# Kernel tuning notes

Measured on AMD Instinct MI355X. Metric: run time of the kernel, lower is better.

The kernel has to match this reference:

```python
import jax, jax.numpy as jnp
import numpy as np

N_LIG, N_TGT, E = 100000, 4000, 150000
D_LIG, D_TGT, H = 4, 1280, 128


def _seg_mean(feat, idx, n):
    # segment mean; isolated nodes get 0 (PyG mean aggr semantics)
    s = jax.ops.segment_sum(feat, idx, num_segments=n)
    c = jax.ops.segment_sum(jnp.ones((idx.shape[0], 1), feat.dtype), idx, num_segments=n)
    return s / jnp.maximum(c, 1.0)


def setup_inputs() -> dict:
    key = jax.random.key(0)
    ks = jax.random.split(key, 20)
    s = 0.05  # weight scale
    inp = {
        'x_ligand': jax.random.normal(ks[0], (N_LIG, D_LIG), jnp.float32),
        'x_target': jax.random.normal(ks[1], (N_TGT, D_TGT), jnp.float32),
        'edge_index': jnp.stack([
            jax.random.randint(ks[2], (E,), 0, N_LIG, jnp.int32),
            jax.random.randint(ks[3], (E,), 0, N_TGT, jnp.int32),
        ]),
        'W1lt_l': jax.random.normal(ks[4], (D_LIG, H), jnp.float32) * s,
        'b1lt':   jax.random.normal(ks[5], (H,), jnp.float32) * s,
        'W1lt_r': jax.random.normal(ks[6], (D_TGT, H), jnp.float32) * s,
        'W1tl_l': jax.random.normal(ks[7], (D_TGT, H), jnp.float32) * s,
        'b1tl':   jax.random.normal(ks[8], (H,), jnp.float32) * s,
        'W1tl_r': jax.random.normal(ks[9], (D_LIG, H), jnp.float32) * s,
        'W2lt_l': jax.random.normal(ks[10], (H, H), jnp.float32) * s,
        'b2lt':   jax.random.normal(ks[11], (H,), jnp.float32) * s,
        'W2lt_r': jax.random.normal(ks[12], (H, H), jnp.float32) * s,
        'W2tl_l': jax.random.normal(ks[13], (H, H), jnp.float32) * s,
        'b2tl':   jax.random.normal(ks[14], (H,), jnp.float32) * s,
        'W2tl_r': jax.random.normal(ks[15], (H, H), jnp.float32) * s,
        'Wp':     jax.random.normal(ks[16], (2 * H, 1), jnp.float32) * s,
        'bp':     jax.random.normal(ks[17], (1,), jnp.float32) * s,
    }
    return inp


def reference(x_ligand, x_target, edge_index,
              W1lt_l, b1lt, W1lt_r, W1tl_l, b1tl, W1tl_r,
              W2lt_l, b2lt, W2lt_r, W2tl_l, b2tl, W2tl_r, Wp, bp):
    src, dst = edge_index[0], edge_index[1]  # ligand idx, target idx

    # conv1: SAGEConv  out = lin_l(mean_j x_src[j]) + lin_r(x_dst)
    m_t = _seg_mean(x_ligand[src], dst, N_TGT)              # [N_TGT, D_LIG]
    h_t = m_t @ W1lt_l + b1lt + x_target @ W1lt_r           # [N_TGT, H]
    m_l = _seg_mean(x_target[dst], src, N_LIG)              # [N_LIG, D_TGT]
    h_l = m_l @ W1tl_l + b1tl + x_ligand @ W1tl_r           # [N_LIG, H]
    h_t = jax.nn.relu(h_t)
    h_l = jax.nn.relu(h_l)

    # conv2 (hidden -> hidden), same edge structure
    m_t2 = _seg_mean(h_l[src], dst, N_TGT)
    h_t2 = jax.nn.relu(m_t2 @ W2lt_l + b2lt + h_t @ W2lt_r)
    m_l2 = _seg_mean(h_t[dst], src, N_LIG)
    h_l2 = jax.nn.relu(m_l2 @ W2tl_l + b2tl + h_l @ W2tl_r)

    # edge predictor: gather-cat-linear
    edge_feats = jnp.concatenate([h_l2[src], h_t2[dst]], axis=-1)  # [E, 2H]
    out = (edge_feats @ Wp + bp).squeeze(-1)                        # [E]
    return out
```

## Files before the change

### kernel.cpp

```cpp
#include <hip/hip_runtime.h>
#include <hip/hip_bf16.h>

#define N_LIG 100000
#define N_TGT 4000
#define NEDGE 150000
#define DT 1280
#define HD 128
#define CAP_L 32
#define CAP_T 128
#define NTILE_L 6250
#define PL_BLOCKS 1563

typedef __attribute__((ext_vector_type(8))) short short8v;
typedef __attribute__((ext_vector_type(4))) float f32x4;

static __device__ __forceinline__ ushort f2bf(float f) {
    __hip_bfloat16 h = __float2bfloat16(f);
    union { __hip_bfloat16 h; ushort u; } c; c.h = h; return c.u;
}
static __device__ __forceinline__ float bf2f(ushort u) {
    union { unsigned v; float f; } c; c.v = ((unsigned)u) << 16; return c.f;
}

__global__ __launch_bounds__(256) void k_pack(
    const float* __restrict__ W2, uint4* __restrict__ Wf,
    const float* __restrict__ Wr, const float* __restrict__ Wl,
    uint4* __restrict__ Wf1,
    const float* __restrict__ xt, uint4* __restrict__ xtf,
    int4* __restrict__ cntz,
    const float* __restrict__ W2a, const float* __restrict__ W2b,
    uint4* __restrict__ Wf2)
{
    int bx = blockIdx.x;
    if (bx < 8) {
        int gid = bx * 256 + threadIdx.x;
        int lane = gid & 63, frag = gid >> 6;
        int ks = frag >> 3, ct = frag & 7;
        int l15 = lane & 15, g = lane >> 4;
        int k = ks * 32 + g * 4, n = ct * 16 + l15;
        union { ushort us[8]; uint4 u; } o;
#pragma unroll
        for (int j = 0; j < 4; ++j) {
            o.us[j]     = f2bf(W2[(size_t)(k + j) * HD + n]);
            o.us[4 + j] = f2bf(W2[(size_t)(k + 16 + j) * HD + n]);
        }
        Wf[gid] = o.u;
    } else if (bx < 168) {
        int gid = (bx - 8) * 256 + threadIdx.x;
        int lane = gid & 63, frag = gid >> 6;
        int ks = frag >> 4, nct = frag & 15;
        int l15 = lane & 15, g = lane >> 4;
        int k = ks * 32 + g * 4, n = nct * 16 + l15;
        const float* Ws = (n < HD) ? Wr : Wl;
        int nn = n & 127;
        union { ushort us[8]; uint4 u; } o;
#pragma unroll
        for (int j = 0; j < 4; ++j) {
            o.us[j]     = f2bf(Ws[(size_t)(k + j) * HD + nn]);
            o.us[4 + j] = f2bf(Ws[(size_t)(k + 16 + j) * HD + nn]);
        }
        Wf1[gid] = o.u;
    } else if (bx < 2668) {
        int gid = (bx - 168) * 256 + threadIdx.x;
        int lane = gid & 63, frag = gid >> 6;
        int ks = frag % 40, rt = frag / 40;
        int row = rt * 16 + (lane & 15);
        int kb = ks * 32 + (lane >> 4) * 4;
        float4 a0 = *reinterpret_cast<const float4*>(xt + (size_t)row * DT + kb);
        float4 a1 = *reinterpret_cast<const float4*>(xt + (size_t)row * DT + kb + 16);
        union { ushort us[8]; uint4 u; } o;
        o.us[0] = f2bf(a0.x); o.us[1] = f2bf(a0.y); o.us[2] = f2bf(a0.z); o.us[3] = f2bf(a0.w);
        o.us[4] = f2bf(a1.x); o.us[5] = f2bf(a1.y); o.us[6] = f2bf(a1.z); o.us[7] = f2bf(a1.w);
        xtf[gid] = o.u;
    } else if (bx < 2770) {
        int i = (bx - 2668) * 256 + threadIdx.x;
        if (i < 26000) cntz[i] = make_int4(0, 0, 0, 0);
    } else {
        int gid = (bx - 2770) * 256 + threadIdx.x;
        int lane = gid & 63, frag = gid >> 6;
        int ks = frag >> 4, nct = frag & 15;
        int l15 = lane & 15, g = lane >> 4;
        int k = ks * 32 + g * 4, n = nct * 16 + l15;
        const float* Ws = (n < HD) ? W2a : W2b;
        int nn = n & 127;
        union { ushort us[8]; uint4 u; } o;
#pragma unroll
        for (int j = 0; j < 4; ++j) {
            o.us[j]     = f2bf(Ws[(size_t)(k + j) * HD + nn]);
            o.us[4 + j] = f2bf(Ws[(size_t)(k + 16 + j) * HD + nn]);
        }
        Wf2[gid] = o.u;
    }
}

__global__ __launch_bounds__(256) void k_fill(
    const int* __restrict__ src, const int* __restrict__ dst,
    int* __restrict__ cnt_src, int* __restrict__ cnt_dst,
    int* __restrict__ bsrc, int* __restrict__ bdst)
{
    int e = blockIdx.x * 256 + threadIdx.x;
    if (e >= NEDGE) return;
    int s = src[e], d = dst[e];
    int ps = atomicAdd(&cnt_src[s], 1);
    if (ps < CAP_L) bsrc[(size_t)s * CAP_L + ps] = d;
    int pd = atomicAdd(&cnt_dst[d], 1);
    if (pd < CAP_T) bdst[(size_t)d * CAP_T + pd] = s;
}

__global__ __launch_bounds__(512) void k_tgt1m(
    const uint4* __restrict__ xtf,
    const uint4* __restrict__ Wf1,
    const uint4* __restrict__ Wf2,
    const float* __restrict__ xl,
    const int* __restrict__ bdst, const int* __restrict__ cnt_dst,
    const float* __restrict__ W1lt_l,
    const float* __restrict__ b1lt,
    float* __restrict__ y_t1,
    float* __restrict__ y_t2, float* __restrict__ htW2r)
{
    __shared__ float  ms[16][4];
    __shared__ ushort hts[16][136];

    int w = threadIdx.x >> 6;
    int lane = threadIdx.x & 63;
    int l15 = lane & 15, g = lane >> 4;
    int rt = blockIdx.x;
    int row0 = rt * 16;

    if (threadIdx.x < 128) {
        int r = threadIdx.x >> 3, lane8 = threadIdx.x & 7;
        int row = row0 + r;
        int deg = cnt_dst[row];
        int n = min(deg, CAP_T);
        float4 acc = make_float4(0.f, 0.f, 0.f, 0.f);
        for (int i = lane8; i < n; i += 8) {
            int sid = bdst[(size_t)row * CAP_T + i];
            float4 x = *reinterpret_cast<const float4*>(xl + 4ull * (unsigned)sid);
            acc.x += x.x; acc.y += x.y; acc.z += x.z; acc.w += x.w;
        }
#pragma unroll
        for (int off = 1; off < 8; off <<= 1) {
            acc.x += __shfl_xor(acc.x, off); acc.y += __shfl_xor(acc.y, off);
            acc.z += __shfl_xor(acc.z, off); acc.w += __shfl_xor(acc.w, off);
        }
        if (lane8 == 0) {
            float dinv = 1.0f / fmaxf((float)deg, 1.0f);
            ms[r][0] = acc.x * dinv; ms[r][1] = acc.y * dinv;
            ms[r][2] = acc.z * dinv; ms[r][3] = acc.w * dinv;
        }
    }

    f32x4 acc[2];
#pragma unroll
    for (int ct = 0; ct < 2; ++ct) acc[ct] = (f32x4){0.f, 0.f, 0.f, 0.f};

    for (int ks = 0; ks < DT / 32; ++ks) {
        union { uint4 u; short8v s; } ua;
        ua.u = xtf[(size_t)(rt * 40 + ks) * 64 + lane];
#pragma unroll
        for (int ct = 0; ct < 2; ++ct) {
            union { uint4 u; short8v s; } ub;
            ub.u = Wf1[(size_t)(ks * 16 + w * 2 + ct) * 64 + lane];
            acc[ct] = __builtin_amdgcn_mfma_f32_16x16x32_bf16(ua.s, ub.s, acc[ct], 0, 0, 0);
        }
    }

    __syncthreads();

    if (w < 4) {
#pragma unroll
        for (int ct = 0; ct < 2; ++ct) {
            int c = w * 32 + ct * 16 + l15;
            float wl0 = W1lt_l[c], wl1 = W1lt_l[HD + c],
                  wl2 = W1lt_l[2 * HD + c], wl3 = W1lt_l[3 * HD + c];
            float bb = b1lt[c];
#pragma unroll
            for (int j = 0; j < 4; ++j) {
                int r = 4 * g + j;
                float v = acc[ct][j] + bb + ms[r][0] * wl0 + ms[r][1] * wl1
                        + ms[r][2] * wl2 + ms[r][3] * wl3;
                hts[r][c] = f2bf(fmaxf(v, 0.0f));
            }
        }
    } else {
#pragma unroll
        for (int ct = 0; ct < 2; ++ct) {
            int c = (w - 4) * 32 + ct * 16 + l15;
#pragma unroll
            for (int j = 0; j < 4; ++j) {
                int grow = row0 + 4 * g + j;
                y_t1[(size_t)grow * HD + c] = acc[ct][j];
            }
        }
    }
    __syncthreads();

    f32x4 acc2[2];
#pragma unroll
    for (int ct = 0; ct < 2; ++ct) acc2[ct] = (f32x4){0.f, 0.f, 0.f, 0.f};

#pragma unroll
    for (int ks2 = 0; ks2 < 4; ++ks2) {
        int kb2 = ks2 * 32 + g * 4;
        union { ushort us[8]; short8v s; } ua2;
        *reinterpret_cast<ushort4*>(&ua2.us[0]) =
            *reinterpret_cast<const ushort4*>(&hts[l15][kb2]);
        *reinterpret_cast<ushort4*>(&ua2.us[4]) =
            *reinterpret_cast<const ushort4*>(&hts[l15][kb2 + 16]);
#pragma unroll
        for (int ct = 0; ct < 2; ++ct) {
            union { uint4 u; short8v s; } ub2;
            ub2.u = Wf2[(size_t)(ks2 * 16 + w * 2 + ct) * 64 + lane];
            acc2[ct] = __builtin_amdgcn_mfma_f32_16x16x32_bf16(ua2.s, ub2.s, acc2[ct], 0, 0, 0);
        }
    }

    float* outp = (w < 4) ? y_t2 : htW2r;
    int cw = (w < 4) ? w : (w - 4);
#pragma unroll
    for (int ct = 0; ct < 2; ++ct) {
        int c = cw * 32 + ct * 16 + l15;
#pragma unroll
        for (int j = 0; j < 4; ++j) {
            int grow = row0 + 4 * g + j;
            outp[(size_t)grow * HD + c] = acc2[ct][j];
        }
    }
}

__global__ __launch_bounds__(256) void k_hl(
    const float* __restrict__ xl,
    const float* __restrict__ y_t1, const float* __restrict__ y_t2,
    const int* __restrict__ bsrc, const int* __restrict__ cnt_src,
    const float* __restrict__ W1tl_r,
    const float* __restrict__ b1tl,
    uint4* __restrict__ hlb,
    uint4* __restrict__ gl2)
{
    int tc = threadIdx.x & 15;
    int node = blockIdx.x * 16 + (threadIdx.x >> 4);
    int ks = tc >> 2, g = tc & 3;
    int kb = ks * 32 + g * 4;

    int deg = cnt_src[node];
    int n = min(deg, CAP_L);
    float4 s0 = make_float4(0.f, 0.f, 0.f, 0.f);
    float4 s1 = make_float4(0.f, 0.f, 0.f, 0.f);
    float4 t0 = make_float4(0.f, 0.f, 0.f, 0.f);
    float4 t1 = make_float4(0.f, 0.f, 0.f, 0.f);
    for (int i = 0; i < n; ++i) {
        int did = bsrc[(size_t)node * CAP_L + i];
        float4 v0 = *reinterpret_cast<const float4*>(y_t1 + (size_t)did * HD + kb);
        float4 v1 = *reinterpret_cast<const float4*>(y_t1 + (size_t)did * HD + kb + 16);
        float4 u0 = *reinterpret_cast<const float4*>(y_t2 + (size_t)did * HD + kb);
        float4 u1 = *reinterpret_cast<const float4*>(y_t2 + (size_t)did * HD + kb + 16);
        s0.x += v0.x; s0.y += v0.y; s0.z += v0.z; s0.w += v0.w;
        s1.x += v1.x; s1.y += v1.y; s1.z += v1.z; s1.w += v1.w;
        t0.x += u0.x; t0.y += u0.y; t0.z += u0.z; t0.w += u0.w;
        t1.x += u1.x; t1.y += u1.y; t1.z += u1.z; t1.w += u1.w;
    }
    float dinv = 1.0f / fmaxf((float)deg, 1.0f);
    float4 x = *reinterpret_cast<const float4*>(xl + 4ull * (unsigned)node);

    float4 b0 = *reinterpret_cast<const float4*>(b1tl + kb);
    float4 b1 = *reinterpret_cast<const float4*>(b1tl + kb + 16);
    float4 wa0 = *reinterpret_cast<const float4*>(W1tl_r + 0 * HD + kb);
    float4 wa1 = *reinterpret_cast<const float4*>(W1tl_r + 1 * HD + kb);
    float4 wa2 = *reinterpret_cast<const float4*>(W1tl_r + 2 * HD + kb);
    float4 wa3 = *reinterpret_cast<const float4*>(W1tl_r + 3 * HD + kb);
    float4 wb0 = *reinterpret_cast<const float4*>(W1tl_r + 0 * HD + kb + 16);
    float4 wb1 = *reinterpret_cast<const float4*>(W1tl_r + 1 * HD + kb + 16);
    float4 wb2 = *reinterpret_cast<const float4*>(W1tl_r + 2 * HD + kb + 16);
    float4 wb3 = *reinterpret_cast<const float4*>(W1tl_r + 3 * HD + kb + 16);

    union { ushort us[8]; uint4 u; } o;
    o.us[0] = f2bf(fmaxf(s0.x * dinv + b0.x + x.x * wa0.x + x.y * wa1.x + x.z * wa2.x + x.w * wa3.x, 0.f));
    o.us[1] = f2bf(fmaxf(s0.y * dinv + b0.y + x.x * wa0.y + x.y * wa1.y + x.z * wa2.y + x.w * wa3.y, 0.f));
    o.us[2] = f2bf(fmaxf(s0.z * dinv + b0.z + x.x * wa0.z + x.y * wa1.z + x.z * wa2.z + x.w * wa3.z, 0.f));
    o.us[3] = f2bf(fmaxf(s0.w * dinv + b0.w + x.x * wa0.w + x.y * wa1.w + x.z * wa2.w + x.w * wa3.w, 0.f));
    o.us[4] = f2bf(fmaxf(s1.x * dinv + b1.x + x.x * wb0.x + x.y * wb1.x + x.z * wb2.x + x.w * wb3.x, 0.f));
    o.us[5] = f2bf(fmaxf(s1.y * dinv + b1.y + x.x * wb0.y + x.y * wb1.y + x.z * wb2.y + x.w * wb3.y, 0.f));
    o.us[6] = f2bf(fmaxf(s1.z * dinv + b1.z + x.x * wb0.z + x.y * wb1.z + x.z * wb2.z + x.w * wb3.z, 0.f));
    o.us[7] = f2bf(fmaxf(s1.w * dinv + b1.w + x.x * wb0.w + x.y * wb1.w + x.z * wb2.w + x.w * wb3.w, 0.f));
    hlb[(size_t)node * 16 + tc] = o.u;

    union { ushort us[8]; uint4 u; } q;
    q.us[0] = f2bf(t0.x * dinv); q.us[1] = f2bf(t0.y * dinv);
    q.us[2] = f2bf(t0.z * dinv); q.us[3] = f2bf(t0.w * dinv);
    q.us[4] = f2bf(t1.x * dinv); q.us[5] = f2bf(t1.y * dinv);
    q.us[6] = f2bf(t1.z * dinv); q.us[7] = f2bf(t1.w * dinv);
    gl2[(size_t)node * 16 + tc] = q.u;
}

__global__ __launch_bounds__(256) void k_ptl(
    const uint4* __restrict__ hlb,
    const uint4* __restrict__ Wf,
    const ushort* __restrict__ gl2,
    const int* __restrict__ bdst, const int* __restrict__ cnt_dst,
    const float* __restrict__ Wlt,
    const float* __restrict__ b2lt,
    const float* __restrict__ b2tl,
    const float* __restrict__ htW2r,
    const float* __restrict__ Wp,
    float* __restrict__ p_t, float* __restrict__ p_l)
{
    __shared__ int   idx[CAP_T];
    __shared__ float sm[16][132];
    __shared__ float msh[HD];
    __shared__ float sum2[2];

    if (blockIdx.x < N_TGT) {
        int row = blockIdx.x;
        int deg = cnt_dst[row];
        int nn = min(deg, CAP_T);

        if (threadIdx.x < CAP_T) idx[threadIdx.x] = bdst[(size_t)row * CAP_T + threadIdx.x];
        __syncthreads();

        int wg = threadIdx.x >> 4, l16 = threadIdx.x & 15;
        float s[8];
#pragma unroll
        for (int j = 0; j < 8; ++j) s[j] = 0.f;
        for (int i = wg; i < nn; i += 16) {
            int sid = idx[i];
            union { uint4 u; ushort us[8]; } v;
            v.u = hlb[(size_t)sid * 16 + l16];
#pragma unroll
            for (int j = 0; j < 8; ++j) s[j] += bf2f(v.us[j]);
        }
#pragma unroll
        for (int j = 0; j < 8; ++j) sm[wg][l16 * 8 + j] = s[j];
        __syncthreads();

        if (threadIdx.x < HD) {
            int h = threadIdx.x;
            int tc2 = h >> 3, jj = h & 7;
            float dinv = 1.0f / fmaxf((float)deg, 1.0f);
            float acc = 0.f;
#pragma unroll
            for (int w2 = 0; w2 < 16; ++w2) acc += sm[w2][tc2 * 8 + jj];
            int ks2 = tc2 >> 2, g2 = tc2 & 3;
            int col = ks2 * 32 + ((jj >> 2) << 4) + g2 * 4 + (jj & 3);
            msh[col] = acc * dinv;
        }
        __syncthreads();

        if (threadIdx.x < HD) {
            int h = threadIdx.x;
            float g = 0.f;
            for (int k = 0; k < HD; k += 4) {
                float4 mk = *reinterpret_cast<const float4*>(&msh[k]);
                g += mk.x * Wlt[(size_t)(k + 0) * HD + h] + mk.y * Wlt[(size_t)(k + 1) * HD + h]
                   + mk.z * Wlt[(size_t)(k + 2) * HD + h] + mk.w * Wlt[(size_t)(k + 3) * HD + h];
            }
            float v = fmaxf(g + b2lt[h] + htW2r[(size_t)row * HD + h], 0.0f);
            float part = v * Wp[HD + h];
#pragma unroll
            for (int off = 1; off < 64; off <<= 1) part += __shfl_xor(part, off);
            if ((h & 63) == 0) sum2[h >> 6] = part;
        }
        __syncthreads();
        if (threadIdx.x == 0) p_t[row] = sum2[0] + sum2[1];
        return;
    }

    int wid = threadIdx.x >> 6;
    int lane = threadIdx.x & 63;
    int l15 = lane & 15, g = lane >> 4;
    int tile = (blockIdx.x - N_TGT) * 4 + wid;
    int wrow0 = tile * 16;

    int arow = wrow0 + l15;
    if (arow >= N_LIG) arow = N_LIG - 1;

    f32x4 acc[8];
#pragma unroll
    for (int ct = 0; ct < 8; ++ct) acc[ct] = (f32x4){0.f, 0.f, 0.f, 0.f};

#pragma unroll
    for (int ks = 0; ks < 4; ++ks) {
        union { uint4 u; short8v s; } ua;
        ua.u = hlb[(size_t)arow * 16 + ks * 4 + g];
#pragma unroll
        for (int ct = 0; ct < 8; ++ct) {
            union { uint4 u; short8v s; } ub;
            ub.u = Wf[(ks * 8 + ct) * 64 + lane];
            acc[ct] = __builtin_amdgcn_mfma_f32_16x16x32_bf16(ua.s, ub.s, acc[ct], 0, 0, 0);
        }
    }

    float wpv[8], bv[8];
    int off8[8];
#pragma unroll
    for (int ct = 0; ct < 8; ++ct) {
        int c = ct * 16 + l15;
        wpv[ct] = Wp[c];
        bv[ct]  = b2tl[c];
        off8[ct] = (((ct >> 1) * 4 + (l15 >> 2)) << 3) + ((ct & 1) << 2) + (l15 & 3);
    }

#pragma unroll
    for (int j = 0; j < 4; ++j) {
        int row = wrow0 + g * 4 + j;
        bool valid = row < N_LIG;
        int lrow = valid ? row : 0;
        const ushort* gp = gl2 + (size_t)lrow * HD;
        float part = 0.f;
#pragma unroll
        for (int ct = 0; ct < 8; ++ct) {
            float v = acc[ct][j] + bf2f(gp[off8[ct]]) + bv[ct];
            part += fmaxf(v, 0.f) * wpv[ct];
        }
#pragma unroll
        for (int off = 1; off < 16; off <<= 1) part += __shfl_xor(part, off);
        if (valid && l15 == 0) p_l[row] = part;
    }
}

__global__ __launch_bounds__(256) void k_out(
    const int* __restrict__ src, const int* __restrict__ dst,
    const float* __restrict__ p_l, const float* __restrict__ p_t,
    const float* __restrict__ bp, float* __restrict__ out)
{
    int e = blockIdx.x * 256 + threadIdx.x;
    if (e >= NEDGE) return;
    out[e] = p_l[src[e]] + p_t[dst[e]] + bp[0];
}

extern "C" void kernel_launch(void* const* d_in, const int* in_sizes, int n_in,
                              void* d_out, int out_size, void* d_ws, size_t ws_size,
                              hipStream_t stream)
{
    const float* x_l    = (const float*)d_in[0];
    const float* x_t    = (const float*)d_in[1];
    const int*   ei     = (const int*)  d_in[2];
    const float* W1lt_l = (const float*)d_in[3];
    const float* b1lt   = (const float*)d_in[4];
    const float* W1lt_r = (const float*)d_in[5];
    const float* W1tl_l = (const float*)d_in[6];
    const float* b1tl   = (const float*)d_in[7];
    const float* W1tl_r = (const float*)d_in[8];
    const float* W2lt_l = (const float*)d_in[9];
    const float* b2lt   = (const float*)d_in[10];
    const float* W2lt_r = (const float*)d_in[11];
    const float* W2tl_l = (const float*)d_in[12];
    const float* b2tl   = (const float*)d_in[13];
    const float* W2tl_r = (const float*)d_in[14];
    const float* Wp     = (const float*)d_in[15];
    const float* bp     = (const float*)d_in[16];

    const int* src = ei;
    const int* dst = ei + NEDGE;

    char* ws = (char*)d_ws;
    size_t o = 0;
    int* cnt_src = (int*)(ws + o); o += (size_t)N_LIG * 4;
    int* cnt_dst = (int*)(ws + o); o += (size_t)N_TGT * 4;
    int* bsrc = (int*)(ws + o); o += (size_t)N_LIG * CAP_L * 4;
    int* bdst = (int*)(ws + o); o += (size_t)N_TGT * CAP_T * 4;
    uint4* hlb   = (uint4*)(ws + o);  o += (size_t)N_LIG * HD * 2;
    uint4* gl2   = (uint4*)(ws + o);  o += (size_t)N_LIG * HD * 2;
    uint4* Wf    = (uint4*)(ws + o);  o += (size_t)32 * 64 * 16;
    uint4* Wf1   = (uint4*)(ws + o);  o += (size_t)640 * 64 * 16;
    uint4* Wf2   = (uint4*)(ws + o);  o += (size_t)64 * 64 * 16;
    uint4* xtf   = (uint4*)(ws + o);  o += (size_t)10000 * 64 * 16;
    float* y_t1  = (float*)(ws + o); o += (size_t)N_TGT * HD * 4;
    float* y_t2  = (float*)(ws + o); o += (size_t)N_TGT * HD * 4;
    float* htW2r = (float*)(ws + o); o += (size_t)N_TGT * HD * 4;
    float* p_l   = (float*)(ws + o); o += (size_t)N_LIG * 4;
    float* p_t   = (float*)(ws + o); o += (size_t)N_TGT * 4;

    float* out = (float*)d_out;

    k_pack<<<2786, 256, 0, stream>>>(W2tl_r, Wf, W1lt_r, W1tl_l, Wf1,
                                     x_t, xtf, (int4*)cnt_src,
                                     W2tl_l, W2lt_r, Wf2);

    k_fill<<<(NEDGE + 255) / 256, 256, 0, stream>>>(src, dst, cnt_src, cnt_dst, bsrc, bdst);

    k_tgt1m<<<N_TGT / 16, 512, 0, stream>>>(xtf, Wf1, Wf2, x_l, bdst, cnt_dst,
                                            W1lt_l, b1lt, y_t1, y_t2, htW2r);

    k_hl<<<NTILE_L, 256, 0, stream>>>(x_l, y_t1, y_t2, bsrc, cnt_src,
                                      W1tl_r, b1tl, hlb, gl2);

    k_ptl<<<N_TGT + PL_BLOCKS, 256, 0, stream>>>(hlb, Wf, (const ushort*)gl2,
                                                 bdst, cnt_dst,
                                                 W2lt_l, b2lt, b2tl, htW2r, Wp,
                                                 p_t, p_l);

    k_out<<<(NEDGE + 255) / 256, 256, 0, stream>>>(src, dst, p_l, p_t, bp, out);
}
```

Before: 107.6 us.

## Fuse ligand conv2 MFMA and predictor dot into the h_l aggregation kernel

The ligand-side conv2 matmul and edge-predictor projection now run in the same kernel that builds h_l and the gathered target mean. The 16-node tile is staged in shared memory and fed to the MFMA there, so the bf16 gl2 buffer is never written to or re-read from global memory. The target-side part moves to its own kernel. Each 16-row tile is now split across four waves by output columns, which needs an extra shared-memory reduction and barriers in a kernel that was previously pure gather.

```diff
diff --git a/kernel.cpp b/kernel.cpp
--- a/kernel.cpp
+++ b/kernel.cpp
@@ -9,7 +9,6 @@
 #define CAP_L 32
 #define CAP_T 128
 #define NTILE_L 6250
-#define PL_BLOCKS 1563
 
 typedef __attribute__((ext_vector_type(8))) short short8v;
 typedef __attribute__((ext_vector_type(4))) float f32x4;
@@ -228,193 +227,200 @@
     }
 }
 
-__global__ __launch_bounds__(256) void k_hl(
+__global__ __launch_bounds__(256) void k_hlp(
     const float* __restrict__ xl,
     const float* __restrict__ y_t1, const float* __restrict__ y_t2,
     const int* __restrict__ bsrc, const int* __restrict__ cnt_src,
     const float* __restrict__ W1tl_r,
     const float* __restrict__ b1tl,
+    const uint4* __restrict__ Wf,
+    const float* __restrict__ b2tl,
+    const float* __restrict__ Wp,
     uint4* __restrict__ hlb,
-    uint4* __restrict__ gl2)
-{
+    float* __restrict__ p_l)
+{
+    __shared__ uint4 Ah[16][17];
+    __shared__ uint4 Gh[16][17];
+    __shared__ float plp[4][16];
+
     int tc = threadIdx.x & 15;
-    int node = blockIdx.x * 16 + (threadIdx.x >> 4);
+    int nd = threadIdx.x >> 4;
+    int node = blockIdx.x * 16 + nd;
     int ks = tc >> 2, g = tc & 3;
     int kb = ks * 32 + g * 4;
 
-    int deg = cnt_src[node];
-    int n = min(deg, CAP_L);
-    float4 s0 = make_float4(0.f, 0.f, 0.f, 0.f);
-    float4 s1 = make_float4(0.f, 0.f, 0.f, 0.f);
-    float4 t0 = make_float4(0.f, 0.f, 0.f, 0.f);
-    float4 t1 = make_float4(0.f, 0.f, 0.f, 0.f);
-    for (int i = 0; i < n; ++i) {
-        int did = bsrc[(size_t)node * CAP_L + i];
-        float4 v0 = *reinterpret_cast<const float4*>(y_t1 + (size_t)did * HD + kb);
-        float4 v1 = *reinterpret_cast<const float4*>(y_t1 + (size_t)did * HD + kb + 16);
-        float4 u0 = *reinterpret_cast<const float4*>(y_t2 + (size_t)did * HD + kb);
-        float4 u1 = *reinterpret_cast<const float4*>(y_t2 + (size_t)did * HD + kb + 16);
-        s0.x += v0.x; s0.y += v0.y; s0.z += v0.z; s0.w += v0.w;
-        s1.x += v1.x; s1.y += v1.y; s1.z += v1.z; s1.w += v1.w;
-        t0.x += u0.x; t0.y += u0.y; t0.z += u0.z; t0.w += u0.w;
-        t1.x += u1.x; t1.y += u1.y; t1.z += u1.z; t1.w += u1.w;
-    }
-    float dinv = 1.0f / fmaxf((float)deg, 1.0f);
-    float4 x = *reinterpret_cast<const float4*>(xl + 4ull * (unsigned)node);
-
-    float4 b0 = *reinterpret_cast<const float4*>(b1tl + kb);
-    float4 b1 = *reinterpret_cast<const float4*>(b1tl + kb + 16);
-    float4 wa0 = *reinterpret_cast<const float4*>(W1tl_r + 0 * HD + kb);
-    float4 wa1 = *reinterpret_cast<const float4*>(W1tl_r + 1 * HD + kb);
-    float4 wa2 = *reinterpret_cast<const float4*>(W1tl_r + 2 * HD + kb);
-    float4 wa3 = *reinterpret_cast<const float4*>(W1tl_r + 3 * HD + kb);
-    float4 wb0 = *reinterpret_cast<const float4*>(W1tl_r + 0 * HD + kb + 16);
-    float4 wb1 = *reinterpret_cast<const float4*>(W1tl_r + 1 * HD + kb + 16);
-    float4 wb2 = *reinterpret_cast<const float4*>(W1tl_r + 2 * HD + kb + 16);
-    float4 wb3 = *reinterpret_cast<const float4*>(W1tl_r + 3 * HD + kb + 16);
-
-    union { ushort us[8]; uint4 u; } o;
-    o.us[0] = f2bf(fmaxf(s0.x * dinv + b0.x + x.x * wa0.x + x.y * wa1.x + x.z * wa2.x + x.w * wa3.x, 0.f));
-    o.us[1] = f2bf(fmaxf(s0.y * dinv + b0.y + x.x * wa0.y + x.y * wa1.y + x.z * wa2.y + x.w * wa3.y, 0.f));
-    o.us[2] = f2bf(fmaxf(s0.z * dinv + b0.z + x.x * wa0.z + x.y * wa1.z + x.z * wa2.z + x.w * wa3.z, 0.f));
-    o.us[3] = f2bf(fmaxf(s0.w * dinv + b0.w + x.x * wa0.w + x.y * wa1.w + x.z * wa2.w + x.w * wa3.w, 0.f));
-    o.us[4] = f2bf(fmaxf(s1.x * dinv + b1.x + x.x * wb0.x + x.y * wb1.x + x.z * wb2.x + x.w * wb3.x, 0.f));
-    o.us[5] = f2bf(fmaxf(s1.y * dinv + b1.y + x.x * wb0.y + x.y * wb1.y + x.z * wb2.y + x.w * wb3.y, 0.f));
-    o.us[6] = f2bf(fmaxf(s1.z * dinv + b1.z + x.x * wb0.z + x.y * wb1.z + x.z * wb2.z + x.w * wb3.z, 0.f));
-    o.us[7] = f2bf(fmaxf(s1.w * dinv + b1.w + x.x * wb0.w + x.y * wb1.w + x.z * wb2.w + x.w * wb3.w, 0.f));
-    hlb[(size_t)node * 16 + tc] = o.u;
-
-    union { ushort us[8]; uint4 u; } q;
-    q.us[0] = f2bf(t0.x * dinv); q.us[1] = f2bf(t0.y * dinv);
-    q.us[2] = f2bf(t0.z * dinv); q.us[3] = f2bf(t0.w * dinv);
-    q.us[4] = f2bf(t1.x * dinv); q.us[5] = f2bf(t1.y * dinv);
-    q.us[6] = f2bf(t1.z * dinv); q.us[7] = f2bf(t1.w * dinv);
-    gl2[(size_t)node * 16 + tc] = q.u;
-}
-
-__global__ __launch_bounds__(256) void k_ptl(
+    {
+        int deg = cnt_src[node];
+        int n = min(deg, CAP_L);
+        float4 s0 = make_float4(0.f, 0.f, 0.f, 0.f);
+        float4 s1 = make_float4(0.f, 0.f, 0.f, 0.f);
+        float4 t0 = make_float4(0.f, 0.f, 0.f, 0.f);
+        float4 t1 = make_float4(0.f, 0.f, 0.f, 0.f);
+        for (int i = 0; i < n; ++i) {
+            int did = bsrc[(size_t)node * CAP_L + i];
+            float4 v0 = *reinterpret_cast<const float4*>(y_t1 + (size_t)did * HD + kb);
+            float4 v1 = *reinterpret_cast<const float4*>(y_t1 + (size_t)did * HD + kb + 16);
+            float4 u0 = *reinterpret_cast<const float4*>(y_t2 + (size_t)did * HD + kb);
+            float4 u1 = *reinterpret_cast<const float4*>(y_t2 + (size_t)did * HD + kb + 16);
+            s0.x += v0.x; s0.y += v0.y; s0.z += v0.z; s0.w += v0.w;
+            s1.x += v1.x; s1.y += v1.y; s1.z += v1.z; s1.w += v1.w;
+            t0.x += u0.x; t0.y += u0.y; t0.z += u0.z; t0.w += u0.w;
+            t1.x += u1.x; t1.y += u1.y; t1.z += u1.z; t1.w += u1.w;
+        }
+        float dinv = 1.0f / fmaxf((float)deg, 1.0f);
+        float4 x = *reinterpret_cast<const float4*>(xl + 4ull * (unsigned)node);
+
+        float4 b0 = *reinterpret_cast<const float4*>(b1tl + kb);
+        float4 b1 = *reinterpret_cast<const float4*>(b1tl + kb + 16);
+        float4 wa0 = *reinterpret_cast<const float4*>(W1tl_r + 0 * HD + kb);
+        float4 wa1 = *reinterpret_cast<const float4*>(W1tl_r + 1 * HD + kb);
+        float4 wa2 = *reinterpret_cast<const float4*>(W1tl_r + 2 * HD + kb);
+        float4 wa3 = *reinterpret_cast<const float4*>(W1tl_r + 3 * HD + kb);
+        float4 wb0 = *reinterpret_cast<const float4*>(W1tl_r + 0 * HD + kb + 16);
+        float4 wb1 = *reinterpret_cast<const float4*>(W1tl_r + 1 * HD + kb + 16);
+        float4 wb2 = *reinterpret_cast<const float4*>(W1tl_r + 2 * HD + kb + 16);
+        float4 wb3 = *reinterpret_cast<const float4*>(W1tl_r + 3 * HD + kb + 16);
+
+        union { ushort us[8]; uint4 u; } o;
+        o.us[0] = f2bf(fmaxf(s0.x * dinv + b0.x + x.x * wa0.x + x.y * wa1.x + x.z * wa2.x + x.w * wa3.x, 0.f));
+        o.us[1] = f2bf(fmaxf(s0.y * dinv + b0.y + x.x * wa0.y + x.y * wa1.y + x.z * wa2.y + x.w * wa3.y, 0.f));
+        o.us[2] = f2bf(fmaxf(s0.z * dinv + b0.z + x.x * wa0.z + x.y * wa1.z + x.z * wa2.z + x.w * wa3.z, 0.f));
+        o.us[3] = f2bf(fmaxf(s0.w * dinv + b0.w + x.x * wa0.w + x.y * wa1.w + x.z * wa2.w + x.w * wa3.w, 0.f));
+        o.us[4] = f2bf(fmaxf(s1.x * dinv + b1.x + x.x * wb0.x + x.y * wb1.x + x.z * wb2.x + x.w * wb3.x, 0.f));
+        o.us[5] = f2bf(fmaxf(s1.y * dinv + b1.y + x.x * wb0.y + x.y * wb1.y + x.z * wb2.y + x.w * wb3.y, 0.f));
+        o.us[6] = f2bf(fmaxf(s1.z * dinv + b1.z + x.x * wb0.z + x.y * wb1.z + x.z * wb2.z + x.w * wb3.z, 0.f));
+        o.us[7] = f2bf(fmaxf(s1.w * dinv + b1.w + x.x * wb0.w + x.y * wb1.w + x.z * wb2.w + x.w * wb3.w, 0.f));
+        hlb[(size_t)node * 16 + tc] = o.u;
+        Ah[nd][tc] = o.u;
+
+        union { ushort us[8]; uint4 u; } q;
+        q.us[0] = f2bf(t0.x * dinv); q.us[1] = f2bf(t0.y * dinv);
+        q.us[2] = f2bf(t0.z * dinv); q.us[3] = f2bf(t0.w * dinv);
+        q.us[4] = f2bf(t1.x * dinv); q.us[5] = f2bf(t1.y * dinv);
+        q.us[6] = f2bf(t1.z * dinv); q.us[7] = f2bf(t1.w * dinv);
+        Gh[nd][tc] = q.u;
+    }
+    __syncthreads();
+
+    int w = threadIdx.x >> 6;
+    int lane = threadIdx.x & 63;
+    int l15 = lane & 15, gq = lane >> 4;
+
+    f32x4 acc[2];
+#pragma unroll
+    for (int c2 = 0; c2 < 2; ++c2) acc[c2] = (f32x4){0.f, 0.f, 0.f, 0.f};
+
+#pragma unroll
+    for (int ksq = 0; ksq < 4; ++ksq) {
+        union { uint4 u; short8v s; } ua;
+        ua.u = Ah[l15][ksq * 4 + gq];
+#pragma unroll
+        for (int c2 = 0; c2 < 2; ++c2) {
+            int ct = w * 2 + c2;
+            union { uint4 u; short8v s; } ub;
+            ub.u = Wf[(ksq * 8 + ct) * 64 + lane];
+            acc[c2] = __builtin_amdgcn_mfma_f32_16x16x32_bf16(ua.s, ub.s, acc[c2], 0, 0, 0);
+        }
+    }
+
+    float wpv[2], bv[2];
+    int off8[2];
+#pragma unroll
+    for (int c2 = 0; c2 < 2; ++c2) {
+        int ct = w * 2 + c2;
+        int c = ct * 16 + l15;
+        wpv[c2] = Wp[c];
+        bv[c2]  = b2tl[c];
+        off8[c2] = (((ct >> 1) * 4 + (l15 >> 2)) << 3) + ((ct & 1) << 2) + (l15 & 3);
+    }
+
+#pragma unroll
+    for (int j = 0; j < 4; ++j) {
+        int r = gq * 4 + j;
+        const ushort* gp = reinterpret_cast<const ushort*>(&Gh[r][0]);
+        float part = 0.f;
+#pragma unroll
+        for (int c2 = 0; c2 < 2; ++c2) {
+            float v = acc[c2][j] + bf2f(gp[off8[c2]]) + bv[c2];
+            part += fmaxf(v, 0.f) * wpv[c2];
+        }
+#pragma unroll
+        for (int off = 1; off < 16; off <<= 1) part += __shfl_xor(part, off);
+        if (l15 == 0) plp[w][r] = part;
+    }
+    __syncthreads();
+
+    if (threadIdx.x < 16) {
+        int r = threadIdx.x;
+        p_l[blockIdx.x * 16 + r] = plp[0][r] + plp[1][r] + plp[2][r] + plp[3][r];
+    }
+}
+
+__global__ __launch_bounds__(256) void k_pt(
     const uint4* __restrict__ hlb,
-    const uint4* __restrict__ Wf,
-    const ushort* __restrict__ gl2,
     const int* __restrict__ bdst, const int* __restrict__ cnt_dst,
     const float* __restrict__ Wlt,
     const float* __restrict__ b2lt,
-    const float* __restrict__ b2tl,
     const float* __restrict__ htW2r,
     const float* __restrict__ Wp,
-    float* __restrict__ p_t, float* __restrict__ p_l)
+    float* __restrict__ p_t)
 {
     __shared__ int   idx[CAP_T];
     __shared__ float sm[16][132];
     __shared__ float msh[HD];
     __shared__ float sum2[2];
 
-    if (blockIdx.x < N_TGT) {
-        int row = blockIdx.x;
-        int deg = cnt_dst[row];
-        int nn = min(deg, CAP_T);
-
-        if (threadIdx.x < CAP_T) idx[threadIdx.x] = bdst[(size_t)row * CAP_T + threadIdx.x];
-        __syncthreads();
-
-        int wg = threadIdx.x >> 4, l16 = threadIdx.x & 15;
-        float s[8];
-#pragma unroll
-        for (int j = 0; j < 8; ++j) s[j] = 0.f;
-        for (int i = wg; i < nn; i += 16) {
-            int sid = idx[i];
-            union { uint4 u; ushort us[8]; } v;
-            v.u = hlb[(size_t)sid * 16 + l16];
-#pragma unroll
-            for (int j = 0; j < 8; ++j) s[j] += bf2f(v.us[j]);
-        }
-#pragma unroll
-        for (int j = 0; j < 8; ++j) sm[wg][l16 * 8 + j] = s[j];
-        __syncthreads();
-
-        if (threadIdx.x < HD) {
-            int h = threadIdx.x;
-            int tc2 = h >> 3, jj = h & 7;
-            float dinv = 1.0f / fmaxf((float)deg, 1.0f);
-            float acc = 0.f;
-#pragma unroll
-            for (int w2 = 0; w2 < 16; ++w2) acc += sm[w2][tc2 * 8 + jj];
-            int ks2 = tc2 >> 2, g2 = tc2 & 3;
-            int col = ks2 * 32 + ((jj >> 2) << 4) + g2 * 4 + (jj & 3);
-            msh[col] = acc * dinv;
-        }
-        __syncthreads();
-
-        if (threadIdx.x < HD) {
-            int h = threadIdx.x;
-            float g = 0.f;
-            for (int k = 0; k < HD; k += 4) {
-                float4 mk = *reinterpret_cast<const float4*>(&msh[k]);
-                g += mk.x * Wlt[(size_t)(k + 0) * HD + h] + mk.y * Wlt[(size_t)(k + 1) * HD + h]
-                   + mk.z * Wlt[(size_t)(k + 2) * HD + h] + mk.w * Wlt[(size_t)(k + 3) * HD + h];
-            }
-            float v = fmaxf(g + b2lt[h] + htW2r[(size_t)row * HD + h], 0.0f);
-            float part = v * Wp[HD + h];
-#pragma unroll
-            for (int off = 1; off < 64; off <<= 1) part += __shfl_xor(part, off);
-            if ((h & 63) == 0) sum2[h >> 6] = part;
-        }
-        __syncthreads();
-        if (threadIdx.x == 0) p_t[row] = sum2[0] + sum2[1];
-        return;
-    }
-
-    int wid = threadIdx.x >> 6;
-    int lane = threadIdx.x & 63;
-    int l15 = lane & 15, g = lane >> 4;
-    int tile = (blockIdx.x - N_TGT) * 4 + wid;
-    int wrow0 = tile * 16;
-
-    int arow = wrow0 + l15;
-    if (arow >= N_LIG) arow = N_LIG - 1;
-
-    f32x4 acc[8];
-#pragma unroll
-    for (int ct = 0; ct < 8; ++ct) acc[ct] = (f32x4){0.f, 0.f, 0.f, 0.f};
-
-#pragma unroll
-    for (int ks = 0; ks < 4; ++ks) {
-        union { uint4 u; short8v s; } ua;
-        ua.u = hlb[(size_t)arow * 16 + ks * 4 + g];
-#pragma unroll
-        for (int ct = 0; ct < 8; ++ct) {
-            union { uint4 u; short8v s; } ub;
-            ub.u = Wf[(ks * 8 + ct) * 64 + lane];
-            acc[ct] = __builtin_amdgcn_mfma_f32_16x16x32_bf16(ua.s, ub.s, acc[ct], 0, 0, 0);
-        }
-    }
-
-    float wpv[8], bv[8];
-    int off8[8];
-#pragma unroll
-    for (int ct = 0; ct < 8; ++ct) {
-        int c = ct * 16 + l15;
-        wpv[ct] = Wp[c];
-        bv[ct]  = b2tl[c];
-        off8[ct] = (((ct >> 1) * 4 + (l15 >> 2)) << 3) + ((ct & 1) << 2) + (l15 & 3);
-    }
-
-#pragma unroll
-    for (int j = 0; j < 4; ++j) {
-        int row = wrow0 + g * 4 + j;
-        bool valid = row < N_LIG;
-        int lrow = valid ? row : 0;
-        const ushort* gp = gl2 + (size_t)lrow * HD;
-        float part = 0.f;
-#pragma unroll
-        for (int ct = 0; ct < 8; ++ct) {
-            float v = acc[ct][j] + bf2f(gp[off8[ct]]) + bv[ct];
-            part += fmaxf(v, 0.f) * wpv[ct];
-        }
-#pragma unroll
-        for (int off = 1; off < 16; off <<= 1) part += __shfl_xor(part, off);
-        if (valid && l15 == 0) p_l[row] = part;
-    }
+    int row = blockIdx.x;
+    int deg = cnt_dst[row];
+    int nn = min(deg, CAP_T);
+
+    if (threadIdx.x < CAP_T) idx[threadIdx.x] = bdst[(size_t)row * CAP_T + threadIdx.x];
+    __syncthreads();
+
+    int wg = threadIdx.x >> 4, l16 = threadIdx.x & 15;
+    float s[8];
+#pragma unroll
+    for (int j = 0; j < 8; ++j) s[j] = 0.f;
+    for (int i = wg; i < nn; i += 16) {
+        int sid = idx[i];
+        union { uint4 u; ushort us[8]; } v;
+        v.u = hlb[(size_t)sid * 16 + l16];
+#pragma unroll
+        for (int j = 0; j < 8; ++j) s[j] += bf2f(v.us[j]);
+    }
+#pragma unroll
+    for (int j = 0; j < 8; ++j) sm[wg][l16 * 8 + j] = s[j];
+    __syncthreads();
+
+    if (threadIdx.x < HD) {
+        int h = threadIdx.x;
+        int tc2 = h >> 3, jj = h & 7;
+        float dinv = 1.0f / fmaxf((float)deg, 1.0f);
+        float acc = 0.f;
+#pragma unroll
+        for (int w2 = 0; w2 < 16; ++w2) acc += sm[w2][tc2 * 8 + jj];
+        int ks2 = tc2 >> 2, g2 = tc2 & 3;
+        int col = ks2 * 32 + ((jj >> 2) << 4) + g2 * 4 + (jj & 3);
+        msh[col] = acc * dinv;
+    }
+    __syncthreads();
+
+    if (threadIdx.x < HD) {
+        int h = threadIdx.x;
+        float g = 0.f;
+        for (int k = 0; k < HD; k += 4) {
+            float4 mk = *reinterpret_cast<const float4*>(&msh[k]);
+            g += mk.x * Wlt[(size_t)(k + 0) * HD + h] + mk.y * Wlt[(size_t)(k + 1) * HD + h]
+               + mk.z * Wlt[(size_t)(k + 2) * HD + h] + mk.w * Wlt[(size_t)(k + 3) * HD + h];
+        }
+        float v = fmaxf(g + b2lt[h] + htW2r[(size_t)row * HD + h], 0.0f);
+        float part = v * Wp[HD + h];
+#pragma unroll
+        for (int off = 1; off < 64; off <<= 1) part += __shfl_xor(part, off);
+        if ((h & 63) == 0) sum2[h >> 6] = part;
+    }
+    __syncthreads();
+    if (threadIdx.x == 0) p_t[row] = sum2[0] + sum2[1];
 }
 
 __global__ __launch_bounds__(256) void k_out(
@@ -459,7 +465,6 @@
     int* bsrc = (int*)(ws + o); o += (size_t)N_LIG * CAP_L * 4;
     int* bdst = (int*)(ws + o); o += (size_t)N_TGT * CAP_T * 4;
     uint4* hlb   = (uint4*)(ws + o);  o += (size_t)N_LIG * HD * 2;
-    uint4* gl2   = (uint4*)(ws + o);  o += (size_t)N_LIG * HD * 2;
     uint4* Wf    = (uint4*)(ws + o);  o += (size_t)32 * 64 * 16;
     uint4* Wf1   = (uint4*)(ws + o);  o += (size_t)640 * 64 * 16;
     uint4* Wf2   = (uint4*)(ws + o);  o += (size_t)64 * 64 * 16;
@@ -481,13 +486,11 @@
     k_tgt1m<<<N_TGT / 16, 512, 0, stream>>>(xtf, Wf1, Wf2, x_l, bdst, cnt_dst,
                                             W1lt_l, b1lt, y_t1, y_t2, htW2r);
 
-    k_hl<<<NTILE_L, 256, 0, stream>>>(x_l, y_t1, y_t2, bsrc, cnt_src,
-                                      W1tl_r, b1tl, hlb, gl2);
-
-    k_ptl<<<N_TGT + PL_BLOCKS, 256, 0, stream>>>(hlb, Wf, (const ushort*)gl2,
-                                                 bdst, cnt_dst,
-                                                 W2lt_l, b2lt, b2tl, htW2r, Wp,
-                                                 p_t, p_l);
+    k_hlp<<<NTILE_L, 256, 0, stream>>>(x_l, y_t1, y_t2, bsrc, cnt_src,
+                                       W1tl_r, b1tl, Wf, b2tl, Wp, hlb, p_l);
+
+    k_pt<<<N_TGT, 256, 0, stream>>>(hlb, bdst, cnt_dst,
+                                    W2lt_l, b2lt, htW2r, Wp, p_t);
 
     k_out<<<(NEDGE + 255) / 256, 256, 0, stream>>>(src, dst, p_l, p_t, bp, out);
 }
```

Measured after the change: 103.5 us. 1.04x faster.
